# Performance work log

Hardware: AMD Instinct MI355X
Metric: run time of the kernel (lower is better)

Reference implementation:

```python
import jax, jax.numpy as jnp
import numpy as np

B, T, I, H, C = 512, 256, 128, 64, 3  # batch, seq_len, input_size, hidden_size, num_classes


def _lstm_dir(x, w_ih, w_hh, b, reverse):
    """Single-direction LSTM over x: (B, T, D_in) -> (B, T, H).

    Gate order matches PyTorch: i, f, g, o. b = b_ih + b_hh (combined).
    Input-to-gate GEMM is hoisted out of the scan for efficiency.
    """
    xg = jnp.einsum('bti,gi->btg', x, w_ih) + b  # (B, T, 4H)
    if reverse:
        xg = xg[:, ::-1]
    xg_t = jnp.swapaxes(xg, 0, 1)  # (T, B, 4H)
    h0 = jnp.zeros((x.shape[0], w_hh.shape[1]), x.dtype)
    c0 = jnp.zeros_like(h0)

    def step(carry, g):
        h, c = carry
        g = g + h @ w_hh.T
        i, f, gg, o = jnp.split(g, 4, axis=-1)
        i = jax.nn.sigmoid(i)
        f = jax.nn.sigmoid(f)
        gg = jnp.tanh(gg)
        o = jax.nn.sigmoid(o)
        c = f * c + i * gg
        h = o * jnp.tanh(c)
        return (h, c), h

    _, hs = jax.lax.scan(step, (h0, c0), xg_t)  # (T, B, H)
    hs = jnp.swapaxes(hs, 0, 1)  # (B, T, H)
    if reverse:
        hs = hs[:, ::-1]
    return hs


def setup_inputs() -> dict:
    key = jax.random.key(0)
    ks = jax.random.split(key, 20)
    s = 1.0 / np.sqrt(H)  # PyTorch LSTM init scale
    d = {"x": jax.random.normal(ks[0], (B, T, I), dtype=jnp.float32)}
    i = 1
    for l, d_in in [(0, I), (1, 2 * H)]:
        for suf in ["f", "r"]:
            d[f"w_ih_l{l}{suf}"] = jax.random.uniform(ks[i], (4 * H, d_in), minval=-s, maxval=s); i += 1
            d[f"w_hh_l{l}{suf}"] = jax.random.uniform(ks[i], (4 * H, H), minval=-s, maxval=s); i += 1
            d[f"b_l{l}{suf}"] = jax.random.uniform(ks[i], (4 * H,), minval=-s, maxval=s); i += 1
    d["fc_w"] = jax.random.uniform(ks[i], (C, 2 * H), minval=-s, maxval=s); i += 1
    d["fc_b"] = jax.random.uniform(ks[i], (C,), minval=-s, maxval=s)
    return d


def reference(x, w_ih_l0f, w_hh_l0f, b_l0f, w_ih_l0r, w_hh_l0r, b_l0r,
              w_ih_l1f, w_hh_l1f, b_l1f, w_ih_l1r, w_hh_l1r, b_l1r,
              fc_w, fc_b):
    # Layer 0 (bidirectional)
    h0f = _lstm_dir(x, w_ih_l0f, w_hh_l0f, b_l0f, False)
    h0r = _lstm_dir(x, w_ih_l0r, w_hh_l0r, b_l0r, True)
    x1 = jnp.concatenate([h0f, h0r], axis=-1)  # (B, T, 2H)
    # (inter-layer dropout is identity in eval mode)
    # Layer 1 (bidirectional)
    h1f = _lstm_dir(x1, w_ih_l1f, w_hh_l1f, b_l1f, False)
    h1r = _lstm_dir(x1, w_ih_l1r, w_hh_l1r, b_l1r, True)
    out = jnp.concatenate([h1f, h1r], axis=-1)  # (B, T, 2H)
    last = out[:, -1, :]  # (B, 2H); dropout is identity in eval mode
    return last @ fc_w.T + fc_b  # (B, C) logits
```

## Files before the change

### kernel.cpp

```cpp
#include <hip/hip_runtime.h>

#define TT 256
#define BB 512
#define NG 256
#define KIN 128

typedef _Float16 half2v __attribute__((ext_vector_type(2)));
typedef _Float16 half4v __attribute__((ext_vector_type(4)));
typedef _Float16 half8v __attribute__((ext_vector_type(8)));
typedef float float4v __attribute__((ext_vector_type(4)));

__device__ __forceinline__ float sig_(float x){ return 1.f/(1.f+__expf(-x)); }
__device__ __forceinline__ float th_(float x){ return fmaf(2.f, 1.f/(1.f+__expf(-2.f*x)), -1.f); }

#if __has_builtin(__builtin_amdgcn_fdot2)
__device__ __forceinline__ float fdot2_(half2v a, half2v b, float c){
  return __builtin_amdgcn_fdot2(a, b, c, false);
}
#else
__device__ __forceinline__ float fdot2_(half2v a, half2v b, float c){
  return c + (float)a[0]*(float)b[0] + (float)a[1]*(float)b[1];
}
#endif

#define SV2(v,k) __builtin_shufflevector((v),(v), 2*(k), 2*(k)+1)

__device__ __forceinline__ half4v ld4h(const float* p){
  float4v v = *reinterpret_cast<const float4v*>(p);
  half4v h; h[0]=(_Float16)v[0]; h[1]=(_Float16)v[1]; h[2]=(_Float16)v[2]; h[3]=(_Float16)v[3];
  return h;
}

__global__ __launch_bounds__(256)
void conv_weights(const float* __restrict__ s0, const float* __restrict__ s1,
                  const float* __restrict__ s2, const float* __restrict__ s3,
                  const float* __restrict__ s4, const float* __restrict__ s5,
                  _Float16* __restrict__ dst)
{
  const int bid = blockIdx.x, tid = threadIdx.x;
  const float* src; int off, idx;
  if (bid < 128)      { src=s0; off=0;      idx=bid*256+tid; }
  else if (bid < 256) { src=s1; off=32768;  idx=(bid-128)*256+tid; }
  else if (bid < 384) { src=s2; off=65536;  idx=(bid-256)*256+tid; }
  else if (bid < 448) { src=s3; off=98304;  idx=(bid-384)*256+tid; }
  else if (bid < 512) { src=s4; off=114688; idx=(bid-448)*256+tid; }
  else                { src=s5; off=131072; idx=(bid-512)*256+tid; }
  dst[off+idx] = (_Float16)src[idx];
}

template<typename AT>
__global__ __launch_bounds__(256)
void gemm_xg(const AT* __restrict__ A, const _Float16* __restrict__ W16,
             const float* __restrict__ bias, _Float16* __restrict__ Cout)
{
  __shared__ __align__(16) _Float16 aL[64][72];
  __shared__ __align__(16) _Float16 wL[256][72];
  const int tid  = threadIdx.x;
  const int wave = tid >> 6;
  const int lane = tid & 63;
  const int lr   = lane & 15;
  const int kg   = lane >> 4;
  const size_t m0 = (size_t)blockIdx.x * 64;

  float4v acc[4][4];
  #pragma unroll
  for (int a=0;a<4;a++)
    #pragma unroll
    for (int b=0;b<4;b++)
      acc[a][b] = float4v{0.f,0.f,0.f,0.f};

  for (int kc = 0; kc < KIN; kc += 64) {
    if constexpr (__is_same(AT, float)) {
      #pragma unroll
      for (int q=0;q<4;q++){
        int fi = tid + q*256;
        int r = fi >> 4, c4 = (fi & 15)*4;
        *reinterpret_cast<half4v*>(&aL[r][c4]) = ld4h(&A[(m0+(size_t)r)*KIN + kc + c4]);
      }
    } else {
      #pragma unroll
      for (int q=0;q<2;q++){
        int fi = tid + q*256;
        int r = fi >> 3, c8 = (fi & 7)*8;
        *reinterpret_cast<half8v*>(&aL[r][c8]) =
            *reinterpret_cast<const half8v*>(&A[(m0+(size_t)r)*KIN + kc + c8]);
      }
    }
    #pragma unroll
    for (int q=0;q<8;q++){
      int fi = tid + q*256;
      int n = fi >> 3, c8 = (fi & 7)*8;
      *reinterpret_cast<half8v*>(&wL[n][c8]) =
          *reinterpret_cast<const half8v*>(&W16[(size_t)n*KIN + kc + c8]);
    }
    __syncthreads();
    #pragma unroll
    for (int ks=0; ks<64; ks+=32){
      half8v af[4], bf[4];
      #pragma unroll
      for (int rt=0;rt<4;rt++)
        af[rt] = *reinterpret_cast<const half8v*>(&aL[rt*16+lr][ks + kg*8]);
      #pragma unroll
      for (int ct=0;ct<4;ct++)
        bf[ct] = *reinterpret_cast<const half8v*>(&wL[wave*64 + ct*16 + lr][ks + kg*8]);
      #pragma unroll
      for (int rt=0;rt<4;rt++)
        #pragma unroll
        for (int ct=0;ct<4;ct++)
          acc[rt][ct] = __builtin_amdgcn_mfma_f32_16x16x32_f16(af[rt], bf[ct], acc[rt][ct], 0,0,0);
    }
    __syncthreads();
  }
  #pragma unroll
  for (int ct=0;ct<4;ct++){
    const int col = wave*64 + ct*16 + lr;
    const float bv = bias[col];
    #pragma unroll
    for (int rt=0;rt<4;rt++){
      const size_t rbase = m0 + rt*16 + kg*4;
      #pragma unroll
      for (int i=0;i<4;i++)
        Cout[(rbase+(size_t)i)*NG + col] = (_Float16)(acc[rt][ct][i] + bv);
    }
  }
}

template<int MODE>
__global__ __launch_bounds__(256, 4)
void lstm_scan_g4(const _Float16* __restrict__ xgPool,
                  const _Float16* __restrict__ whhPool,
                  int nF,
                  _Float16* __restrict__ x1out, float* __restrict__ hfin)
{
  const int tid = threadIdx.x;
  const int w   = tid >> 6;
  const int j   = tid & 63;
  const bool rev = (int)blockIdx.x >= nF;
  const int b = rev ? ((int)blockIdx.x - nF) : (int)blockIdx.x;
  const _Float16* xg  = xgPool  + (rev ? (size_t)BB*TT*NG : 0);
  const _Float16* whh = whhPool + (rev ? (size_t)16384 : 0);

  __shared__ __align__(16) float acts[2][256];
  __shared__ __align__(16) _Float16 hs4[4][64];

  half8v wreg[8];
  #pragma unroll
  for (int q=0;q<8;q++)
    wreg[q] = *reinterpret_cast<const half8v*>(&whh[(size_t)(w*64 + j)*64 + q*8]);

  hs4[w][j] = (_Float16)0.f;
  float c = 0.f, h_last = 0.f;

  const _Float16* xgb = xg + (size_t)b*TT*NG + w*64 + j;
  _Float16 ring[8];
  #pragma unroll
  for (int u=0;u<8;u++)
    ring[u] = xgb[(size_t)(rev ? (TT-1-u) : u) * NG];

  for (int tb=0; tb<TT; tb+=8){
    #pragma unroll
    for (int u=0;u<8;u++){
      const int tt = tb + u;
      const int t  = rev ? (TT-1-tt) : tt;

      const float xp = (float)ring[u];
      const int tf = tt + 8;
      if (tf < TT)
        ring[u] = xgb[(size_t)(rev ? (TT-1-tf) : tf) * NG];

      float a=0.f, a2=0.f;
      #pragma unroll
      for (int q=0;q<8;q++){
        const half8v h8 = *reinterpret_cast<const half8v*>(&hs4[w][q*8]);
        a  = fdot2_(SV2(wreg[q],0), SV2(h8,0), a);
        a2 = fdot2_(SV2(wreg[q],1), SV2(h8,1), a2);
        a  = fdot2_(SV2(wreg[q],2), SV2(h8,2), a);
        a2 = fdot2_(SV2(wreg[q],3), SV2(h8,3), a2);
      }
      const float pre = xp + (a + a2);
      acts[tt&1][w*64 + j] = (w==2) ? th_(pre) : sig_(pre);
      __syncthreads();

      const float iv = acts[tt&1][j];
      const float fv = acts[tt&1][64+j];
      const float gv = acts[tt&1][128+j];
      const float ov = acts[tt&1][192+j];
      c = fv*c + iv*gv;
      const float h = ov * th_(c);
      h_last = h;
      hs4[w][j] = (_Float16)h;
      if constexpr (MODE==0)
        if (w == 0)
          x1out[((size_t)b*TT + t)*128 + (rev ? 64 : 0) + j] = (_Float16)h;
    }
  }
  if constexpr (MODE==1)
    if (w == 0)
      hfin[(size_t)b*64 + j] = h_last;
}

__global__ __launch_bounds__(256)
void final_fuse(const _Float16* __restrict__ x1, const float* __restrict__ w_ih,
                const float* __restrict__ bvec, const float* __restrict__ hfin,
                const float* __restrict__ fcw, const float* __restrict__ fcb,
                float* __restrict__ out)
{
  const int b = blockIdx.x, tid = threadIdx.x;
  __shared__ float xs[128];
  __shared__ float act[256];
  __shared__ float hall[128];
  if (tid < 128) xs[tid] = (float)x1[((size_t)b*TT + (TT-1))*128 + tid];
  __syncthreads();
  float a = bvec[tid];
  #pragma unroll
  for (int kk=0;kk<32;kk++){
    float4v wv = *reinterpret_cast<const float4v*>(&w_ih[(size_t)tid*128 + kk*4]);
    a += wv[0]*xs[kk*4] + wv[1]*xs[kk*4+1] + wv[2]*xs[kk*4+2] + wv[3]*xs[kk*4+3];
  }
  const int grp = tid>>6;
  act[tid] = (grp==2) ? th_(a) : sig_(a);
  __syncthreads();
  if (tid < 64) {
    float c = act[tid]*act[128+tid];
    float h = act[192+tid]*th_(c);
    hall[64+tid] = h;
    hall[tid] = hfin[(size_t)b*64 + tid];
  }
  __syncthreads();
  if (tid < 3) {
    float acc2 = fcb[tid];
    for (int k=0;k<128;k++) acc2 += fcw[(size_t)tid*128 + k]*hall[k];
    out[(size_t)b*3 + tid] = acc2;
  }
}

extern "C" void kernel_launch(void* const* d_in, const int* in_sizes, int n_in,
                              void* d_out, int out_size, void* d_ws, size_t ws_size,
                              hipStream_t stream) {
  const float* x        = (const float*)d_in[0];
  const float* w_ih_l0f = (const float*)d_in[1];
  const float* w_hh_l0f = (const float*)d_in[2];
  const float* b_l0f    = (const float*)d_in[3];
  const float* w_ih_l0r = (const float*)d_in[4];
  const float* w_hh_l0r = (const float*)d_in[5];
  const float* b_l0r    = (const float*)d_in[6];
  const float* w_ih_l1f = (const float*)d_in[7];
  const float* w_hh_l1f = (const float*)d_in[8];
  const float* b_l1f    = (const float*)d_in[9];
  const float* w_ih_l1r = (const float*)d_in[10];
  const float* b_l1r    = (const float*)d_in[12];
  const float* fc_w     = (const float*)d_in[13];
  const float* fc_b     = (const float*)d_in[14];
  float* out = (float*)d_out;

  const size_t XG_BYTES = (size_t)BB*TT*NG*2;
  const size_t X1_BYTES = (size_t)BB*TT*128*2;
  const size_t HF_BYTES = (size_t)BB*64*4;
  const size_t W16_BYTES = (size_t)147456*2;
  if (ws_size < 2*XG_BYTES + X1_BYTES + HF_BYTES + W16_BYTES) return;
  _Float16* xgF  = (_Float16*)d_ws;
  _Float16* xgR  = (_Float16*)((char*)d_ws + XG_BYTES);
  _Float16* x1   = (_Float16*)((char*)d_ws + 2*XG_BYTES);
  float*    hfin = (float*)   ((char*)d_ws + 2*XG_BYTES + X1_BYTES);
  _Float16* w16  = (_Float16*)((char*)d_ws + 2*XG_BYTES + X1_BYTES + HF_BYTES);
  _Float16* wih_l0f16 = w16;
  _Float16* wih_l0r16 = w16 + 32768;
  _Float16* wih_l1f16 = w16 + 65536;
  _Float16* whh_l0f16 = w16 + 98304;
  _Float16* whh_l1f16 = w16 + 131072;

  const int MBLK = (BB*TT)/64;

  conv_weights<<<576, 256, 0, stream>>>(w_ih_l0f, w_ih_l0r, w_ih_l1f,
                                        w_hh_l0f, w_hh_l0r, w_hh_l1f, w16);
  gemm_xg<float><<<MBLK, 256, 0, stream>>>(x, wih_l0f16, b_l0f, xgF);
  gemm_xg<float><<<MBLK, 256, 0, stream>>>(x, wih_l0r16, b_l0r, xgR);
  lstm_scan_g4<0><<<1024, 256, 0, stream>>>(xgF, whh_l0f16, 512, x1, nullptr);
  gemm_xg<_Float16><<<MBLK, 256, 0, stream>>>(x1, wih_l1f16, b_l1f, xgF);
  lstm_scan_g4<1><<<512, 256, 0, stream>>>(xgF, whh_l1f16, 512, nullptr, hfin);
  final_fuse<<<BB, 256, 0, stream>>>(x1, w_ih_l1r, b_l1r, hfin, fc_w, fc_b, out);
}
```

Before: 402.8 us.

## Process two batch rows per block in layer-0 LSTM scan to share weights and barriers

The layer-0 scan kernel now handles two batch rows per 256-thread block, reusing the register-resident recurrent weights for both rows and paying one barrier per timestep for both. This halves the grid for layer 0 (512 blocks instead of 1024) and doubles the dot-product work per thread. Pointer-increment addressing replaces per-step index math. The cost is more registers and LDS per block and a longer serial chain per thread, which may reduce latency hiding.

After: 528.1 us. 1.31x slower.

```diff
diff --git a/kernel.cpp b/kernel.cpp
--- a/kernel.cpp
+++ b/kernel.cpp
@@ -125,78 +125,122 @@
   }
 }
 
-template<int MODE>
+template<int NR, int MODE>
 __global__ __launch_bounds__(256, 4)
-void lstm_scan_g4(const _Float16* __restrict__ xgPool,
-                  const _Float16* __restrict__ whhPool,
-                  int nF,
-                  _Float16* __restrict__ x1out, float* __restrict__ hfin)
+void lstm_scan_d(const _Float16* __restrict__ xgPool,
+                 const _Float16* __restrict__ whhPool,
+                 int nF,
+                 _Float16* __restrict__ x1out, float* __restrict__ hfin)
 {
   const int tid = threadIdx.x;
   const int w   = tid >> 6;
   const int j   = tid & 63;
   const bool rev = (int)blockIdx.x >= nF;
-  const int b = rev ? ((int)blockIdx.x - nF) : (int)blockIdx.x;
+  const int bblk = rev ? ((int)blockIdx.x - nF) : (int)blockIdx.x;
+  const int r0 = bblk * NR;
   const _Float16* xg  = xgPool  + (rev ? (size_t)BB*TT*NG : 0);
   const _Float16* whh = whhPool + (rev ? (size_t)16384 : 0);
 
-  __shared__ __align__(16) float acts[2][256];
-  __shared__ __align__(16) _Float16 hs4[4][64];
+  __shared__ __align__(16) float acts[2][NR][256];
+  __shared__ __align__(16) _Float16 hs4[4][NR][64];
 
   half8v wreg[8];
   #pragma unroll
   for (int q=0;q<8;q++)
-    wreg[q] = *reinterpret_cast<const half8v*>(&whh[(size_t)(w*64 + j)*64 + q*8]);
-
-  hs4[w][j] = (_Float16)0.f;
-  float c = 0.f, h_last = 0.f;
-
-  const _Float16* xgb = xg + (size_t)b*TT*NG + w*64 + j;
-  _Float16 ring[8];
-  #pragma unroll
-  for (int u=0;u<8;u++)
-    ring[u] = xgb[(size_t)(rev ? (TT-1-u) : u) * NG];
+    wreg[q] = *reinterpret_cast<const half8v*>(&whh[(size_t)tid*64 + q*8]);
+
+  hs4[w][0][j] = (_Float16)0.f;
+  if constexpr (NR==2) hs4[w][1][j] = (_Float16)0.f;
+  float c0 = 0.f, c1 = 0.f, hl0 = 0.f, hl1 = 0.f;
+  __syncthreads();
+
+  const ptrdiff_t dT = rev ? -(ptrdiff_t)NG : (ptrdiff_t)NG;
+  const int tstart = rev ? (TT-1) : 0;
+  const _Float16* pa0 = xg + ((size_t)(r0+0)*TT + tstart)*NG + tid;
+  const _Float16* pa1 = (NR==2) ? (xg + ((size_t)(r0+1)*TT + tstart)*NG + tid) : pa0;
+
+  _Float16 rg0[8], rg1[8];
+  #pragma unroll
+  for (int u=0;u<8;u++){
+    rg0[u] = *pa0; pa0 += dT;
+    if constexpr (NR==2){ rg1[u] = *pa1; pa1 += dT; }
+  }
+
+  const ptrdiff_t dX = rev ? -(ptrdiff_t)128 : (ptrdiff_t)128;
+  const int xoff = rev ? 64 : 0;
+  _Float16* q0 = (MODE==0) ? x1out + ((size_t)(r0+0)*TT + tstart)*128 + xoff + j : nullptr;
+  _Float16* q1 = (MODE==0 && NR==2) ? x1out + ((size_t)(r0+1)*TT + tstart)*128 + xoff + j : nullptr;
 
   for (int tb=0; tb<TT; tb+=8){
     #pragma unroll
     for (int u=0;u<8;u++){
       const int tt = tb + u;
-      const int t  = rev ? (TT-1-tt) : tt;
-
-      const float xp = (float)ring[u];
-      const int tf = tt + 8;
-      if (tf < TT)
-        ring[u] = xgb[(size_t)(rev ? (TT-1-tf) : tf) * NG];
-
-      float a=0.f, a2=0.f;
+      const int par = tt & 1;
+
+      const float xp0 = (float)rg0[u];
+      float xp1 = 0.f;
+      if constexpr (NR==2) xp1 = (float)rg1[u];
+      if (tt+8 < TT){
+        rg0[u] = *pa0; pa0 += dT;
+        if constexpr (NR==2){ rg1[u] = *pa1; pa1 += dT; }
+      }
+
+      float a0=0.f, b0=0.f, a1=0.f, b1=0.f;
       #pragma unroll
       for (int q=0;q<8;q++){
-        const half8v h8 = *reinterpret_cast<const half8v*>(&hs4[w][q*8]);
-        a  = fdot2_(SV2(wreg[q],0), SV2(h8,0), a);
-        a2 = fdot2_(SV2(wreg[q],1), SV2(h8,1), a2);
-        a  = fdot2_(SV2(wreg[q],2), SV2(h8,2), a);
-        a2 = fdot2_(SV2(wreg[q],3), SV2(h8,3), a2);
-      }
-      const float pre = xp + (a + a2);
-      acts[tt&1][w*64 + j] = (w==2) ? th_(pre) : sig_(pre);
+        const half8v w8 = wreg[q];
+        const half8v h80 = *reinterpret_cast<const half8v*>(&hs4[w][0][q*8]);
+        a0 = fdot2_(SV2(w8,0), SV2(h80,0), a0);
+        b0 = fdot2_(SV2(w8,1), SV2(h80,1), b0);
+        a0 = fdot2_(SV2(w8,2), SV2(h80,2), a0);
+        b0 = fdot2_(SV2(w8,3), SV2(h80,3), b0);
+        if constexpr (NR==2){
+          const half8v h81 = *reinterpret_cast<const half8v*>(&hs4[w][1][q*8]);
+          a1 = fdot2_(SV2(w8,0), SV2(h81,0), a1);
+          b1 = fdot2_(SV2(w8,1), SV2(h81,1), b1);
+          a1 = fdot2_(SV2(w8,2), SV2(h81,2), a1);
+          b1 = fdot2_(SV2(w8,3), SV2(h81,3), b1);
+        }
+      }
+      const float pre0 = xp0 + (a0 + b0);
+      acts[par][0][tid] = (w==2) ? th_(pre0) : sig_(pre0);
+      if constexpr (NR==2){
+        const float pre1 = xp1 + (a1 + b1);
+        acts[par][1][tid] = (w==2) ? th_(pre1) : sig_(pre1);
+      }
       __syncthreads();
 
-      const float iv = acts[tt&1][j];
-      const float fv = acts[tt&1][64+j];
-      const float gv = acts[tt&1][128+j];
-      const float ov = acts[tt&1][192+j];
-      c = fv*c + iv*gv;
-      const float h = ov * th_(c);
-      h_last = h;
-      hs4[w][j] = (_Float16)h;
-      if constexpr (MODE==0)
-        if (w == 0)
-          x1out[((size_t)b*TT + t)*128 + (rev ? 64 : 0) + j] = (_Float16)h;
-    }
-  }
-  if constexpr (MODE==1)
-    if (w == 0)
-      hfin[(size_t)b*64 + j] = h_last;
+      {
+        const float iv = acts[par][0][j];
+        const float fv = acts[par][0][64+j];
+        const float gv = acts[par][0][128+j];
+        const float ov = acts[par][0][192+j];
+        c0 = fv*c0 + iv*gv;
+        const float h = ov * th_(c0);
+        hl0 = h;
+        hs4[w][0][j] = (_Float16)h;
+        if constexpr (MODE==0)
+          if (w == 0){ *q0 = (_Float16)h; q0 += dX; }
+      }
+      if constexpr (NR==2){
+        const float iv = acts[par][1][j];
+        const float fv = acts[par][1][64+j];
+        const float gv = acts[par][1][128+j];
+        const float ov = acts[par][1][192+j];
+        c1 = fv*c1 + iv*gv;
+        const float h = ov * th_(c1);
+        hl1 = h;
+        hs4[w][1][j] = (_Float16)h;
+        if constexpr (MODE==0)
+          if (w == 1){ *q1 = (_Float16)h; q1 += dX; }
+      }
+    }
+  }
+  if constexpr (MODE==1){
+    if (w == 0) hfin[(size_t)(r0+0)*64 + j] = hl0;
+    if constexpr (NR==2)
+      if (w == 1) hfin[(size_t)(r0+1)*64 + j] = hl1;
+  }
 }
 
 __global__ __launch_bounds__(256)
@@ -275,8 +319,8 @@
                                         w_hh_l0f, w_hh_l0r, w_hh_l1f, w16);
   gemm_xg<float><<<MBLK, 256, 0, stream>>>(x, wih_l0f16, b_l0f, xgF);
   gemm_xg<float><<<MBLK, 256, 0, stream>>>(x, wih_l0r16, b_l0r, xgR);
-  lstm_scan_g4<0><<<1024, 256, 0, stream>>>(xgF, whh_l0f16, 512, x1, nullptr);
+  lstm_scan_d<2,0><<<512, 256, 0, stream>>>(xgF, whh_l0f16, 256, x1, nullptr);
   gemm_xg<_Float16><<<MBLK, 256, 0, stream>>>(x1, wih_l1f16, b_l1f, xgF);
-  lstm_scan_g4<1><<<512, 256, 0, stream>>>(xgF, whh_l1f16, 512, nullptr, hfin);
+  lstm_scan_d<1,1><<<512, 256, 0, stream>>>(xgF, whh_l1f16, 512, nullptr, hfin);
   final_fuse<<<BB, 256, 0, stream>>>(x1, w_ih_l1r, b_l1r, hfin, fc_w, fc_b, out);
 }
```
